# Optimization experiments

Hardware: AMD Instinct MI355X
Metric: run time of the kernel (lower is better)

The kernel has to match this reference:

```python
import jax, jax.numpy as jnp
import numpy as np

DIM, HK, HV, DK, DV, KC = 2048, 16, 32, 128, 128, 4
B, L = 1, 8192
EPS = 1e-6


def setup_inputs() -> dict:
    key = jax.random.key(0)
    ks = jax.random.split(key, 12)
    conv_dim = 2 * HK * DK + HV * DV  # 8192
    inp = {
        "x": jax.random.normal(ks[0], (B, L, DIM), jnp.float32),
        "cu_seqlens": jnp.array([0, 2048, 4096, 6144, 8192], jnp.int64),
        "Wqkv": jax.random.normal(ks[1], (DIM, conv_dim), jnp.float32) * 0.02,
        "Wz": jax.random.normal(ks[2], (DIM, HV * DV), jnp.float32) * 0.02,
        "Wa": jax.random.normal(ks[3], (DIM, HV), jnp.float32) * 0.02,
        "Wb": jax.random.normal(ks[4], (DIM, HV), jnp.float32) * 0.02,
        "conv_w": jax.random.normal(ks[5], (conv_dim, KC), jnp.float32) * 0.2,
        "A_log": jnp.zeros((HV,), jnp.float32),
        "dt_bias": jnp.ones((HV,), jnp.float32),
        "norm_w": jnp.ones((DV,), jnp.float32),
        "Wout": jax.random.normal(ks[6], (HV * DV, DIM), jnp.float32) * 0.02,
    }
    return inp


def _causal_conv_silu(qkv, conv_w, seq_idx):
    # depthwise causal conv1d with per-sequence masking (channels-last)
    Bb, Ll, C = qkv.shape
    xp = jnp.pad(qkv, ((0, 0), (KC - 1, 0), (0, 0)))
    sp = jnp.pad(seq_idx, ((0, 0), (KC - 1, 0)), constant_values=-1)
    out = jnp.zeros_like(qkv)
    for i in range(KC):
        m = (sp[:, i:i + Ll] == seq_idx)[..., None]
        out = out + conv_w[:, i] * jnp.where(m, xp[:, i:i + Ll], 0.0)
    return jax.nn.silu(out)


def _l2norm(x):
    return x * jax.lax.rsqrt(jnp.sum(x * x, axis=-1, keepdims=True) + EPS)


def reference(x, cu_seqlens, Wqkv, Wz, Wa, Wb, conv_w, A_log, dt_bias, norm_w, Wout):
    Bb, Ll, _ = x.shape
    qkv = x @ Wqkv            # [B,L,conv_dim]
    z = x @ Wz                # [B,L,HV*DV]
    a = x @ Wa                # [B,L,HV]
    b = x @ Wb                # [B,L,HV]

    pos = jnp.arange(Ll)
    seq_idx = jnp.searchsorted(cu_seqlens[1:-1], pos, side="right").astype(jnp.int32)
    seq_idx = jnp.broadcast_to(seq_idx[None, :], (Bb, Ll))

    mixed = _causal_conv_silu(qkv, conv_w, seq_idx)
    key_dim, value_dim = HK * DK, HV * DV
    q, k, v = jnp.split(mixed, [key_dim, 2 * key_dim], axis=-1)
    q = q.reshape(Bb, Ll, HK, DK)
    k = k.reshape(Bb, Ll, HK, DK)
    v = v.reshape(Bb, Ll, HV, DV)
    rep = HV // HK
    q = jnp.repeat(q, rep, axis=2)  # [B,L,HV,DK]
    k = jnp.repeat(k, rep, axis=2)

    # gates
    g = -jnp.exp(A_log) * jax.nn.softplus(a + dt_bias)   # [B,L,HV] (log decay)
    beta = jax.nn.sigmoid(b)                              # [B,L,HV]

    # l2-normed q/k, q scaled
    q = _l2norm(q) * (DK ** -0.5)
    k = _l2norm(k)

    # sequence-start flags for state reset
    starts = jnp.zeros((Ll,), bool).at[cu_seqlens[:-1]].set(True)

    def step(S, inp):
        q_t, k_t, v_t, g_t, b_t, s_t = inp
        S = jnp.where(s_t, 0.0, S)
        S = S * jnp.exp(g_t)[..., None, None]                 # decay
        kv = jnp.einsum("bhk,bhkv->bhv", k_t, S)              # S^T k
        delta = (v_t - kv) * b_t[..., None]
        S = S + k_t[..., :, None] * delta[..., None, :]       # rank-1 delta update
        o = jnp.einsum("bhk,bhkv->bhv", q_t, S)
        return S, o

    S0 = jnp.zeros((Bb, HV, DK, DV), q.dtype)
    xs = (jnp.moveaxis(q, 1, 0), jnp.moveaxis(k, 1, 0), jnp.moveaxis(v, 1, 0),
          jnp.moveaxis(g, 1, 0), jnp.moveaxis(beta, 1, 0), starts)
    _, o = jax.lax.scan(step, S0, xs)                          # [L,B,HV,DV]
    o = jnp.moveaxis(o, 0, 1)                                  # [B,L,HV,DV]

    # gated RMSNorm (gate applied before norm, swish)
    zh = z.reshape(Bb, Ll, HV, DV)
    y = o * jax.nn.silu(zh)
    y = y * jax.lax.rsqrt(jnp.mean(y * y, axis=-1, keepdims=True) + EPS) * norm_w

    return y.reshape(Bb, Ll, HV * DV) @ Wout
```

## Files before the change

### kernel.cpp

```cpp
#include <hip/hip_runtime.h>
#include <hip/hip_bf16.h>
#include <stdint.h>
#include <stdio.h>

#define L_SEQ 8192
#define DIM_ 2048
#define HK_ 16
#define HV_ 32
#define DK_ 128
#define DV_ 128
#define CONV_DIM_ 8192
#define EPS_F 1e-6f

typedef __bf16 bf16;
typedef __bf16 bf16x8 __attribute__((ext_vector_type(8)));
typedef __bf16 bf16x4 __attribute__((ext_vector_type(4)));
typedef __bf16 bf16x2 __attribute__((ext_vector_type(2)));
typedef float f32x4 __attribute__((ext_vector_type(4)));

__device__ __forceinline__ void load_lds16(const void* g, void* l) {
  __builtin_amdgcn_global_load_lds((const __attribute__((address_space(1))) uint32_t*)g,
                                   (__attribute__((address_space(3))) uint32_t*)l,
                                   16, 0, 0);
}

__global__ __launch_bounds__(256) void k_convert(const float4* __restrict__ src,
                                                 bf16x4* __restrict__ dst, int n4) {
#pragma unroll
  for (int it = 0; it < 8; it++) {
    int i = blockIdx.x * 2048 + it * 256 + threadIdx.x;
    if (i >= n4) continue;
    float4 v = src[i];
    bf16x4 o;
    o[0] = (bf16)v.x; o[1] = (bf16)v.y; o[2] = (bf16)v.z; o[3] = (bf16)v.w;
    dst[i] = o;
  }
}

__global__ __launch_bounds__(256) void k_transpose_cvt(const float* __restrict__ W,
                                                       bf16* __restrict__ Wt, int K, int ldW,
                                                       int n_off) {
  __shared__ float tile[32][33];
  int n0 = blockIdx.x * 32, k0 = blockIdx.y * 32;
  int cx = threadIdx.x & 31, ry = threadIdx.x >> 5;
#pragma unroll
  for (int i = 0; i < 4; i++)
    tile[ry + i * 8][cx] = W[(size_t)(k0 + ry + i * 8) * ldW + n_off + n0 + cx];
  __syncthreads();
#pragma unroll
  for (int i = 0; i < 4; i++) {
    int r = ry + i * 8;
    Wt[(size_t)(n0 + r) * K + k0 + cx] = (bf16)tile[cx][r];
  }
}

template <int BF16_OUT>
__global__ __launch_bounds__(256) void k_gemm_bt(const bf16* __restrict__ A,
                                                 const bf16* __restrict__ Bt,
                                                 void* __restrict__ Cout,
                                                 int M, int N, int K) {
  __shared__ __align__(16) bf16 la[4096];
  __shared__ __align__(16) bf16 lb[4096];
  const int tid = threadIdx.x;
  const int lane = tid & 63;
  const int wave = tid >> 6;
  const int wm = wave >> 1, wn = wave & 1;
  const int bm = blockIdx.y << 7, bn = blockIdx.x << 7;

  f32x4 acc[4][4];
#pragma unroll
  for (int i = 0; i < 4; i++)
#pragma unroll
    for (int j = 0; j < 4; j++) acc[i][j] = (f32x4){0.f, 0.f, 0.f, 0.f};

  const bf16* Ag = A + (size_t)(bm + lane) * K + wave * 8;
  const bf16* Bg = Bt + (size_t)(bn + lane) * K + wave * 8;
  bf16* lA = la + wave * 1024;
  bf16* lB = lb + wave * 1024;
  const size_t rowskip = (size_t)64 * K;

  const int chunk = lane >> 4;
  const int rr = lane & 15;
  const bf16* fa = la + chunk * 1024 + (wm * 64 + rr) * 8;
  const bf16* fb = lb + chunk * 1024 + (wn * 64 + rr) * 8;

  for (int k0 = 0; k0 < K; k0 += 32) {
    __syncthreads();
    load_lds16(Ag + k0, lA);
    load_lds16(Ag + k0 + rowskip, lA + 512);
    load_lds16(Bg + k0, lB);
    load_lds16(Bg + k0 + rowskip, lB + 512);
    __syncthreads();
    bf16x8 af[4], bfr[4];
#pragma unroll
    for (int i = 0; i < 4; i++) {
      af[i] = *(const bf16x8*)(fa + i * 16 * 8);
      bfr[i] = *(const bf16x8*)(fb + i * 16 * 8);
    }
#pragma unroll
    for (int mi = 0; mi < 4; mi++)
#pragma unroll
      for (int ni = 0; ni < 4; ni++)
        acc[mi][ni] = __builtin_amdgcn_mfma_f32_16x16x32_bf16(af[mi], bfr[ni], acc[mi][ni], 0, 0, 0);
  }

  const int col = bn + wn * 64 + rr;
  const int row0 = bm + wm * 64 + (lane >> 4) * 4;
#pragma unroll
  for (int mi = 0; mi < 4; mi++)
#pragma unroll
    for (int ni = 0; ni < 4; ni++)
#pragma unroll
      for (int r = 0; r < 4; r++) {
        int rowi = row0 + mi * 16 + r;
        int coli = col + ni * 16;
        if (BF16_OUT)
          ((bf16*)Cout)[(size_t)rowi * N + coli] = (bf16)acc[mi][ni][r];
        else
          ((float*)Cout)[(size_t)rowi * N + coli] = acc[mi][ni][r];
      }
}

__global__ __launch_bounds__(256) void k_gates(const float* __restrict__ x,
                                               const float* __restrict__ Wa,
                                               const float* __restrict__ Wb,
                                               const float* __restrict__ A_log,
                                               const float* __restrict__ dt_bias,
                                               float* __restrict__ gb) {
  int t = blockIdx.x * 4 + (threadIdx.x >> 6);
  int lane = threadIdx.x & 63;
  int h = lane & 31;
  int isB = lane >> 5;
  const float* W = isB ? Wb : Wa;
  const float* xr = x + (size_t)t * DIM_;
  float a0 = 0.f, a1 = 0.f, a2 = 0.f, a3 = 0.f;
  for (int kk = 0; kk < DIM_; kk += 4) {
    float4 xv = *(const float4*)(xr + kk);
    a0 += xv.x * W[(kk + 0) * 32 + h];
    a1 += xv.y * W[(kk + 1) * 32 + h];
    a2 += xv.z * W[(kk + 2) * 32 + h];
    a3 += xv.w * W[(kk + 3) * 32 + h];
  }
  float acc = (a0 + a1) + (a2 + a3);
  if (isB) {
    gb[(size_t)t * 64 + 32 + h] = 1.f / (1.f + expf(-acc));
  } else {
    float ag = acc + dt_bias[h];
    float sp = (ag > 20.f) ? ag : log1pf(expf(ag));
    gb[(size_t)t * 64 + h] = -expf(A_log[h]) * sp;
  }
}

template <int IS_V>
__global__ __launch_bounds__(128) void k_conv(const bf16* __restrict__ src,
                                              const float* __restrict__ conv_w,
                                              const int* __restrict__ cu, int nseq,
                                              bf16* __restrict__ qn, bf16* __restrict__ kn,
                                              bf16* __restrict__ v) {
  __shared__ float red[2];
  const int grp = blockIdx.y;
  const int c = grp * 128 + threadIdx.x;
  float4 w = *(const float4*)(conv_w + (size_t)(c + (IS_V ? 4096 : 0)) * 4);
  for (int it = 0; it < 8; it++) {
    int t = blockIdx.x * 8 + it;
    int start = 0;
    for (int s = 0; s < nseq; s++) {
      int a = cu[s];
      if (a <= t) start = a;
    }
    float accv = 0.f;
#pragma unroll
    for (int i = 0; i < 4; i++) {
      int tp = t - 3 + i;
      if (tp >= start) {
        float wv = (i == 0) ? w.x : (i == 1) ? w.y : (i == 2) ? w.z : w.w;
        accv += wv * (float)src[(size_t)tp * 4096 + c];
      }
    }
    float val = accv / (1.f + __expf(-accv));
    if (IS_V) {
      v[((size_t)t * HV_ + grp) * DV_ + threadIdx.x] = (bf16)val;
    } else {
      float ss = val * val;
#pragma unroll
      for (int off = 1; off < 64; off <<= 1) ss += __shfl_xor(ss, off);
      if ((threadIdx.x & 63) == 0) red[threadIdx.x >> 6] = ss;
      __syncthreads();
      float tot = red[0] + red[1];
      float scale = rsqrtf(tot + EPS_F);
      if (grp < 16) {
        scale *= 0.08838834764831845f;
        qn[((size_t)t * HK_ + grp) * DK_ + threadIdx.x] = (bf16)(val * scale);
      } else {
        kn[((size_t)t * HK_ + (grp - 16)) * DK_ + threadIdx.x] = (bf16)(val * scale);
      }
      __syncthreads();
    }
  }
}


#define SA_LD 68
#define SUF_LD 65

__device__ __forceinline__ bf16x8 frag256(const bf16* base, int tile, int kk, int lane) {
  int row = tile * 16 + (lane & 15);
  int blk = kk * 4 + (lane >> 4);
  int byte = row * 256 + (((blk & 8) | ((blk & 7) ^ (row & 7))) << 4);
  return *(const bf16x8*)((const char*)base + byte);
}
__device__ __forceinline__ bf16x8 frag128(const bf16* base, int tile, int kk, int lane) {
  int row = tile * 16 + (lane & 15);
  int blk = kk * 4 + (lane >> 4);
  int byte = row * 128 + ((blk ^ (row & 7)) << 4);
  return *(const bf16x8*)((const char*)base + byte);
}
__device__ __forceinline__ bf16x8 ld256v(const bf16* base, int row, int blk) {
  int byte = row * 256 + (((blk & 8) | ((blk & 7) ^ (row & 7))) << 4);
  return *(const bf16x8*)((const char*)base + byte);
}
__device__ __forceinline__ void st128e(bf16* base, int row, int col, float v) {
  int byte = row * 128 + ((((col >> 3) ^ (row & 7)) << 4)) + (col & 7) * 2;
  *(bf16*)((char*)base + byte) = (bf16)v;
}
__device__ __forceinline__ float ld128e(const bf16* base, int row, int col) {
  int byte = row * 128 + ((((col >> 3) ^ (row & 7)) << 4)) + (col & 7) * 2;
  return (float)*(const bf16*)((const char*)base + byte);
}
__device__ __forceinline__ void st256e(bf16* base, int row, int col, float v) {
  int blk = col >> 3;
  int byte = row * 256 + (((blk & 8) | ((blk & 7) ^ (row & 7))) << 4) + (col & 7) * 2;
  *(bf16*)((char*)base + byte) = (bf16)v;
}

__global__ __launch_bounds__(512, 2) void k_scan_chunk(const bf16* __restrict__ qn,
                                                       const bf16* __restrict__ kn,
                                                       const bf16* __restrict__ v,
                                                       const float* __restrict__ gb,
                                                       const int* __restrict__ cu,
                                                       bf16* __restrict__ o) {
  __shared__ __align__(16) bf16 sK[64 * 128];
  __shared__ __align__(16) bf16 sQ[64 * 128];
  __shared__ __align__(16) bf16 sKt[128 * 64];
  __shared__ __align__(16) bf16 sSt[64 * 128];
  __shared__ __align__(16) bf16 sV[64 * 64];
  __shared__ __align__(16) bf16 sM[64 * 64];
  __shared__ __align__(16) bf16 sUt[64 * 64];
  __shared__ float sA[64 * SA_LD];
  __shared__ float sUf[64 * SUF_LD];
  __shared__ float sG2[2][64], sB[2][64], sEg[2][64];

  const int h = blockIdx.y;
  const int hk = h >> 1;
  const int seq = blockIdx.z;
  const int dv0 = blockIdx.x * 64;
  const int tid = threadIdx.x;
  const int lane = tid & 63;
  const int wave = tid >> 6;
  const int w4 = wave & 3;
  const int grp = wave >> 2;
  const int t0 = cu[seq], t1 = cu[seq + 1];
  if (t0 >= t1) return;

  f32x4 St[4];
#pragma unroll
  for (int c = 0; c < 4; c++) St[c] = (f32x4){0.f, 0.f, 0.f, 0.f};
  ((float4*)sSt)[tid] = (float4){0.f, 0.f, 0.f, 0.f};
  ((float4*)sSt)[tid + 512] = (float4){0.f, 0.f, 0.f, 0.f};

  auto stageKQV = [&](int ts) {
#pragma unroll
    for (int it = 0; it < 2; it++) {
      int Bx = (wave * 2 + it) * 64 + lane;
      int r = Bx >> 4, bq = Bx & 15;
      int tr = ts + r; if (tr >= t1) tr = t1 - 1;
      int bs = (bq & 8) | ((bq & 7) ^ (r & 7));
      size_t go = (size_t)tr * (HK_ * DK_) + hk * DK_ + bs * 8;
      load_lds16(kn + go, (char*)sK + (size_t)(wave * 2 + it) * 1024);
      load_lds16(qn + go, (char*)sQ + (size_t)(wave * 2 + it) * 1024);
    }
    {
      int Bx = wave * 64 + lane;
      int r = Bx >> 3, bq = Bx & 7;
      int tr = ts + r; if (tr >= t1) tr = t1 - 1;
      int bs = bq ^ (r & 7);
      load_lds16(v + (size_t)tr * (HV_ * DV_) + h * DV_ + dv0 + bs * 8,
                 (char*)sV + (size_t)wave * 1024);
    }
  };

  auto prefix = [&](int ts, int pb) {
    int tr = ts + lane;
    float gv = 0.f, bv = 0.f;
    if (tr < t1) {
      gv = gb[(size_t)tr * 64 + h] * 1.44269504088896f;
      bv = gb[(size_t)tr * 64 + 32 + h];
    }
    float ps = gv;
#pragma unroll
    for (int off = 1; off < 64; off <<= 1) {
      float tmp = __shfl_up(ps, off);
      if (lane >= off) ps += tmp;
    }
    sG2[pb][lane] = ps;
    sB[pb][lane] = bv;
    sEg[pb][lane] = exp2f(ps);
  };

  int buf = 0;
  stageKQV(t0);
  if (wave == 0) prefix(t0, 0);
  __syncthreads();

  bool first = true;
  for (int ts = t0; ts < t1; ts += 64) {
    const bool haveNext = (ts + 64 < t1);
    const float* G2 = sG2[buf];
    const float* Bt = sB[buf];
    const float* Eg = sEg[buf];

    f32x4 accA[4], accB[4];
#pragma unroll
    for (int c = 0; c < 4; c++) {
      accA[c] = (f32x4){0.f, 0.f, 0.f, 0.f};
      accB[c] = (f32x4){0.f, 0.f, 0.f, 0.f};
    }
    const bf16* opA = grp ? sK : sQ;
#pragma unroll
    for (int kk = 0; kk < 4; kk++) {
      bf16x8 af = frag256(opA, w4, kk, lane);
#pragma unroll
      for (int c = 0; c < 4; c++) {
        if (c <= w4) {
          bf16x8 bk = frag256(sK, c, kk, lane);
          accA[c] = __builtin_amdgcn_mfma_f32_16x16x32_bf16(af, bk, accA[c], 0, 0, 0);
        }
        if (!first) {
          bf16x8 bs_ = frag256(sSt, c, kk, lane);
          accB[c] = __builtin_amdgcn_mfma_f32_16x16x32_bf16(af, bs_, accB[c], 0, 0, 0);
        }
      }
    }

    const float G2c = G2[63];
    const int li = lane & 15, lh = lane >> 4;
    {
      float g2s[4];
#pragma unroll
      for (int c = 0; c < 4; c++) g2s[c] = G2[c * 16 + li];
      if (grp) {
#pragma unroll
        for (int r = 0; r < 4; r++) {
          const int t = w4 * 16 + lh * 4 + r;
          const float g2t = G2[t], btv = Bt[t], egt = Eg[t];
#pragma unroll
          for (int c = 0; c < 4; c++) {
            const int s = c * 16 + li;
            const float e = exp2f(g2t - g2s[c]);
            sA[t * SA_LD + s] = (s < t) ? btv * e * accA[c][r] : 0.f;
            sUf[t * SUF_LD + s] = btv * (ld128e(sV, t, s) - egt * accB[c][r]);
          }
        }
      } else {
#pragma unroll
        for (int r = 0; r < 4; r++) {
          const int t = w4 * 16 + lh * 4 + r;
          const float g2t = G2[t];
#pragma unroll
          for (int c = 0; c < 4; c++) {
            const int s = c * 16 + li;
            const float e = exp2f(g2t - g2s[c]);
            st128e(sM, t, s, (s <= t) ? e * accA[c][r] : 0.f);
          }
        }
        const int tt = lane;
        const float sc = exp2f(G2c - G2[tt]);
#pragma unroll
        for (int i = 0; i < 4; i++) {
          int dk0 = w4 * 32 + i * 8;
          bf16x8 kv = ld256v(sK, tt, w4 * 4 + i);
#pragma unroll
          for (int j = 0; j < 8; j++) st128e(sKt, dk0 + j, tt, (float)kv[j] * sc);
        }
      }
    }
    __syncthreads();

    if (haveNext) {
      stageKQV(ts + 64);
      if (wave == 7) prefix(ts + 64, buf ^ 1);
    }

    for (int b = 0; b < 4; b++) {
      if (wave == 0) {
        const int b16o = b * 16;
        float u[16];
#pragma unroll
        for (int i = 0; i < 16; i++) {
          const int t = b16o + i;
          float x = sUf[t * SUF_LD + lane];
          const float* Ar = &sA[t * SA_LD + b16o];
#pragma unroll
          for (int j = 0; j < i; j++) x -= Ar[j] * u[j];
          u[i] = x;
          sUf[t * SUF_LD + lane] = x;
        }
      }
      __syncthreads();
      if (b < 3) {
        if (wave >= 1 && wave <= 6) {
          const int b16o = b * 16;
          float us[16];
#pragma unroll
          for (int j = 0; j < 16; j++) us[j] = sUf[(b16o + j) * SUF_LD + lane];
          for (int t = b16o + 16 + (wave - 1); t < 64; t += 6) {
            float x = sUf[t * SUF_LD + lane];
            const float* Ar = &sA[t * SA_LD + b16o];
#pragma unroll
            for (int j = 0; j < 16; j++) x -= Ar[j] * us[j];
            sUf[t * SUF_LD + lane] = x;
          }
        }
        __syncthreads();
      }
    }

    {
      const int s = lane;
#pragma unroll
      for (int i = 0; i < 8; i++) {
        int dvv = wave * 8 + i;
        st128e(sUt, dvv, s, sUf[s * SUF_LD + dvv]);
      }
    }
    __syncthreads();

    if (!grp) {
      f32x4 aO[4];
#pragma unroll
      for (int c = 0; c < 4; c++)
#pragma unroll
        for (int r = 0; r < 4; r++)
          aO[c][r] = Eg[w4 * 16 + lh * 4 + r] * accB[c][r];
#pragma unroll
      for (int kk = 0; kk < 2; kk++) {
        bf16x8 am = frag128(sM, w4, kk, lane);
#pragma unroll
        for (int c = 0; c < 4; c++) {
          bf16x8 bu = frag128(sUt, c, kk, lane);
          aO[c] = __builtin_amdgcn_mfma_f32_16x16x32_bf16(am, bu, aO[c], 0, 0, 0);
        }
      }
#pragma unroll
      for (int r = 0; r < 4; r++) {
        const int t = w4 * 16 + lh * 4 + r;
        if (ts + t < t1) {
#pragma unroll
          for (int c = 0; c < 4; c++)
            o[((size_t)(ts + t) * HV_ + h) * DV_ + dv0 + c * 16 + li] = (bf16)aO[c][r];
        }
      }
    }

    {
      const float egc = Eg[63];
#pragma unroll
      for (int c = 0; c < 4; c++)
#pragma unroll
        for (int r = 0; r < 4; r++) St[c][r] *= egc;
#pragma unroll
      for (int kk = 0; kk < 2; kk++) {
        bf16x8 akt = frag128(sKt, wave, kk, lane);
#pragma unroll
        for (int c = 0; c < 4; c++) {
          bf16x8 bu = frag128(sUt, c, kk, lane);
          St[c] = __builtin_amdgcn_mfma_f32_16x16x32_bf16(akt, bu, St[c], 0, 0, 0);
        }
      }
#pragma unroll
      for (int c = 0; c < 4; c++)
#pragma unroll
        for (int r = 0; r < 4; r++) {
          int dk = wave * 16 + lh * 4 + r;
          int dvv = c * 16 + li;
          st256e(sSt, dvv, dk, St[c][r]);
        }
    }
    first = false;
    buf ^= 1;
    __syncthreads();
  }
}

__global__ __launch_bounds__(256) void k_gatenorm(const bf16* __restrict__ o,
                                                  const bf16* __restrict__ z,
                                                  const float* __restrict__ norm_w,
                                                  bf16* __restrict__ y) {
  int lane = threadIdx.x & 63;
  int i0 = lane * 2;
  float2 nw = *(const float2*)(norm_w + i0);
#pragma unroll
  for (int it = 0; it < 16; it++) {
    int row = blockIdx.x * 64 + it * 4 + (threadIdx.x >> 6);
    bf16x2 ov = *(const bf16x2*)(o + (size_t)row * 128 + i0);
    bf16x2 zv = *(const bf16x2*)(z + (size_t)row * 128 + i0);
    float zf0 = (float)zv[0], zf1 = (float)zv[1];
    float y0 = (float)ov[0] * (zf0 / (1.f + __expf(-zf0)));
    float y1 = (float)ov[1] * (zf1 / (1.f + __expf(-zf1)));
    float ss = y0 * y0 + y1 * y1;
#pragma unroll
    for (int off = 1; off < 64; off <<= 1) ss += __shfl_xor(ss, off);
    float scale = rsqrtf(ss * (1.f / 128.f) + EPS_F);
    bf16x2 out;
    out[0] = (bf16)(y0 * scale * nw.x);
    out[1] = (bf16)(y1 * scale * nw.y);
    *(bf16x2*)(y + (size_t)row * 128 + i0) = out;
  }
}

extern "C" void kernel_launch(void* const* d_in, const int* in_sizes, int n_in,
                              void* d_out, int out_size, void* d_ws, size_t ws_size,
                              hipStream_t stream) {
  const float* x = (const float*)d_in[0];
  const int* cu = (const int*)d_in[1];
  const float* Wqkv = (const float*)d_in[2];
  const float* Wz = (const float*)d_in[3];
  const float* Wa = (const float*)d_in[4];
  const float* Wb = (const float*)d_in[5];
  const float* conv_w = (const float*)d_in[6];
  const float* A_log = (const float*)d_in[7];
  const float* dt_bias = (const float*)d_in[8];
  const float* norm_w = (const float*)d_in[9];
  const float* Wout = (const float*)d_in[10];
  float* out = (float*)d_out;
  const int nseq = in_sizes[1] - 1;

  const size_t MB = 1024 * 1024;
  char* ws = (char*)d_ws;
  bf16* x16   = (bf16*)(ws + 0);
  bf16* WtS   = (bf16*)(ws + 32 * MB);
  bf16* qn    = (bf16*)(ws + 48 * MB);
  bf16* kn    = (bf16*)(ws + 80 * MB);
  bf16* bigA  = (bf16*)(ws + 112 * MB);
  bf16* vbuf  = (bf16*)(ws + 176 * MB);
  float* gb   = (float*)(ws + 240 * MB);
  bf16* z16   = qn;
  bf16* o16   = bigA;
  bf16* y16   = z16;

  if (242 * MB > ws_size) {
    fprintf(stderr, "WORKSPACE TOO SMALL: need %zu, have %zu\n", 242 * MB, ws_size);
    return;
  }

  k_convert<<<L_SEQ * DIM_ / 4 / 2048, 256, 0, stream>>>((const float4*)x, (bf16x4*)x16,
                                                         L_SEQ * DIM_ / 4);
  k_gates<<<L_SEQ / 4, 256, 0, stream>>>(x, Wa, Wb, A_log, dt_bias, gb);

  k_transpose_cvt<<<dim3(4096 / 32, DIM_ / 32), 256, 0, stream>>>(Wqkv, WtS, DIM_, CONV_DIM_, 0);
  k_gemm_bt<1><<<dim3(4096 / 128, L_SEQ / 128), 256, 0, stream>>>(x16, WtS, bigA, L_SEQ, 4096, DIM_);
  k_conv<0><<<dim3(L_SEQ / 8, 32), 128, 0, stream>>>(bigA, conv_w, cu, nseq, qn, kn, vbuf);

  k_transpose_cvt<<<dim3(4096 / 32, DIM_ / 32), 256, 0, stream>>>(Wqkv, WtS, DIM_, CONV_DIM_, 4096);
  k_gemm_bt<1><<<dim3(4096 / 128, L_SEQ / 128), 256, 0, stream>>>(x16, WtS, bigA, L_SEQ, 4096, DIM_);
  k_conv<1><<<dim3(L_SEQ / 8, 32), 128, 0, stream>>>(bigA, conv_w, cu, nseq, qn, kn, vbuf);

  k_scan_chunk<<<dim3(2, HV_, nseq), 512, 0, stream>>>(qn, kn, vbuf, gb, cu, o16);

  k_transpose_cvt<<<dim3(4096 / 32, DIM_ / 32), 256, 0, stream>>>(Wz, WtS, DIM_, 4096, 0);
  k_gemm_bt<1><<<dim3(4096 / 128, L_SEQ / 128), 256, 0, stream>>>(x16, WtS, z16, L_SEQ, 4096, DIM_);

  k_gatenorm<<<L_SEQ * HV_ / 64, 256, 0, stream>>>(o16, z16, norm_w, y16);

  k_transpose_cvt<<<dim3(DIM_ / 32, 4096 / 32), 256, 0, stream>>>(Wout, WtS, 4096, DIM_, 0);
  k_gemm_bt<0><<<dim3(DIM_ / 128, L_SEQ / 128), 256, 0, stream>>>(y16, WtS, out, L_SEQ, DIM_, 4096);
}
```

Measured before the change: 2.139 ms.

## Replace scalar chunk triangular solve with register shuffles and MFMA block updates

The within-chunk triangular solve (UT transform) no longer runs as scalar fp32 loops over shared-memory matrices. Each 16-row block is solved in registers by one wave using shuffles, and the trailing off-diagonal updates use bf16 MFMA against the negated A matrix stored in LDS. This removes the large fp32 sA/sUf buffers and several synchronisation passes, but the intermediate U blocks are rounded to bf16 before feeding later blocks, which may cost accuracy. The GEMM also gains an XCD-aware workgroup swizzle so neighbouring tiles share L2.

```diff
diff --git a/kernel.cpp b/kernel.cpp
--- a/kernel.cpp
+++ b/kernel.cpp
@@ -65,7 +65,13 @@
   const int lane = tid & 63;
   const int wave = tid >> 6;
   const int wm = wave >> 1, wn = wave & 1;
-  const int bm = blockIdx.y << 7, bn = blockIdx.x << 7;
+
+  const int gx = gridDim.x;
+  const int nwg = gx * gridDim.y;
+  const int lid = blockIdx.y * gx + blockIdx.x;
+  const int cpx = nwg >> 3;
+  const int swz = (lid & 7) * cpx + (lid >> 3);
+  const int bm = (swz / gx) << 7, bn = (swz % gx) << 7;
 
   f32x4 acc[4][4];
 #pragma unroll
@@ -200,9 +206,6 @@
 }
 
 
-#define SA_LD 68
-#define SUF_LD 65
-
 __device__ __forceinline__ bf16x8 frag256(const bf16* base, int tile, int kk, int lane) {
   int row = tile * 16 + (lane & 15);
   int blk = kk * 4 + (lane >> 4);
@@ -212,6 +215,12 @@
 __device__ __forceinline__ bf16x8 frag128(const bf16* base, int tile, int kk, int lane) {
   int row = tile * 16 + (lane & 15);
   int blk = kk * 4 + (lane >> 4);
+  int byte = row * 128 + ((blk ^ (row & 7)) << 4);
+  return *(const bf16x8*)((const char*)base + byte);
+}
+__device__ __forceinline__ bf16x8 frag128w(const bf16* base, int tile, int blkbase, int lane) {
+  int row = tile * 16 + (lane & 15);
+  int blk = blkbase + (lane >> 4);
   int byte = row * 128 + ((blk ^ (row & 7)) << 4);
   return *(const bf16x8*)((const char*)base + byte);
 }
@@ -246,8 +255,7 @@
   __shared__ __align__(16) bf16 sV[64 * 64];
   __shared__ __align__(16) bf16 sM[64 * 64];
   __shared__ __align__(16) bf16 sUt[64 * 64];
-  __shared__ float sA[64 * SA_LD];
-  __shared__ float sUf[64 * SUF_LD];
+  __shared__ __align__(16) bf16 sAb[64 * 64];
   __shared__ float sG2[2][64], sB[2][64], sEg[2][64];
 
   const int h = blockIdx.y;
@@ -318,6 +326,7 @@
     const float* G2 = sG2[buf];
     const float* Bt = sB[buf];
     const float* Eg = sEg[buf];
+    const int li = lane & 15, lh = lane >> 4;
 
     f32x4 accA[4], accB[4];
 #pragma unroll
@@ -342,8 +351,8 @@
       }
     }
 
+    ((float4*)sUt)[tid] = (float4){0.f, 0.f, 0.f, 0.f};
     const float G2c = G2[63];
-    const int li = lane & 15, lh = lane >> 4;
     {
       float g2s[4];
 #pragma unroll
@@ -357,8 +366,10 @@
           for (int c = 0; c < 4; c++) {
             const int s = c * 16 + li;
             const float e = exp2f(g2t - g2s[c]);
-            sA[t * SA_LD + s] = (s < t) ? btv * e * accA[c][r] : 0.f;
-            sUf[t * SUF_LD + s] = btv * (ld128e(sV, t, s) - egt * accB[c][r]);
+            float am = (s < t) ? btv * e * accA[c][r] : 0.f;
+            accA[c][r] = am;
+            st128e(sAb, t, s, -am);
+            accB[c][r] = btv * (ld128e(sV, t, s) - egt * accB[c][r]);
           }
         }
       } else {
@@ -388,52 +399,40 @@
 
     if (haveNext) {
       stageKQV(ts + 64);
-      if (wave == 7) prefix(ts + 64, buf ^ 1);
-    }
-
+      if (wave == 3) prefix(ts + 64, buf ^ 1);
+    }
+
+#pragma unroll
     for (int b = 0; b < 4; b++) {
-      if (wave == 0) {
-        const int b16o = b * 16;
-        float u[16];
-#pragma unroll
-        for (int i = 0; i < 16; i++) {
-          const int t = b16o + i;
-          float x = sUf[t * SUF_LD + lane];
-          const float* Ar = &sA[t * SA_LD + b16o];
-#pragma unroll
-          for (int j = 0; j < i; j++) x -= Ar[j] * u[j];
-          u[i] = x;
-          sUf[t * SUF_LD + lane] = x;
-        }
+      if (wave == 4 + b) {
+#pragma unroll
+        for (int j = 0; j < 16; j++) {
+          float ub[4], av[4];
+#pragma unroll
+          for (int c = 0; c < 4; c++) ub[c] = __shfl(accB[c][j & 3], ((j >> 2) << 4) | li);
+#pragma unroll
+          for (int r = 0; r < 4; r++) av[r] = __shfl(accA[b][r], (lh << 4) | j);
+#pragma unroll
+          for (int r = 0; r < 4; r++)
+#pragma unroll
+            for (int c = 0; c < 4; c++) accB[c][r] -= av[r] * ub[c];
+        }
+#pragma unroll
+        for (int c = 0; c < 4; c++)
+#pragma unroll
+          for (int r = 0; r < 4; r++)
+            st128e(sUt, c * 16 + li, b * 16 + lh * 4 + r, accB[c][r]);
       }
       __syncthreads();
-      if (b < 3) {
-        if (wave >= 1 && wave <= 6) {
-          const int b16o = b * 16;
-          float us[16];
-#pragma unroll
-          for (int j = 0; j < 16; j++) us[j] = sUf[(b16o + j) * SUF_LD + lane];
-          for (int t = b16o + 16 + (wave - 1); t < 64; t += 6) {
-            float x = sUf[t * SUF_LD + lane];
-            const float* Ar = &sA[t * SA_LD + b16o];
-#pragma unroll
-            for (int j = 0; j < 16; j++) x -= Ar[j] * us[j];
-            sUf[t * SUF_LD + lane] = x;
-          }
-        }
-        __syncthreads();
-      }
-    }
-
-    {
-      const int s = lane;
-#pragma unroll
-      for (int i = 0; i < 8; i++) {
-        int dvv = wave * 8 + i;
-        st128e(sUt, dvv, s, sUf[s * SUF_LD + dvv]);
-      }
-    }
-    __syncthreads();
+      if (b < 3 && grp == 1 && w4 > b) {
+        bf16x8 af = frag128w(sAb, w4, b * 2, lane);
+#pragma unroll
+        for (int c = 0; c < 4; c++) {
+          bf16x8 uf = frag128w(sUt, c, b * 2, lane);
+          accB[c] = __builtin_amdgcn_mfma_f32_16x16x32_bf16(af, uf, accB[c], 0, 0, 0);
+        }
+      }
+    }
 
     if (!grp) {
       f32x4 aO[4];
```

Measured after the change: 2.159 ms. Within noise of the previous version (+0.9%).
